# Performance work log

Measured on AMD Instinct MI355X. Metric: run time of the kernel, lower is better.

Reference implementation:

```python
import jax, jax.numpy as jnp
import numpy as np

N_ARY = 4
H_SIZE = 512
X_SIZE = 512
DEPTH = 9
N_NODES = (N_ARY ** DEPTH - 1) // (N_ARY - 1)  # 87381, complete 4-ary tree, BFS numbering


def setup_inputs() -> dict:
    key = jax.random.key(0)
    ks = jax.random.split(key, 7)
    x = jax.random.normal(ks[0], (N_NODES, X_SIZE), jnp.float32)
    # torch nn.Linear convention: y = x @ W.T + b, W:[out, in]
    Ww = jax.random.normal(ks[1], (H_SIZE, X_SIZE), jnp.float32) * (X_SIZE ** -0.5)
    Wb = jax.random.normal(ks[2], (H_SIZE,), jnp.float32) * 0.01
    Uzr_w = jax.random.normal(ks[3], (2 * H_SIZE, N_ARY * H_SIZE), jnp.float32) * ((N_ARY * H_SIZE) ** -0.5)
    Uzr_b = jax.random.normal(ks[4], (2 * H_SIZE,), jnp.float32) * 0.01
    Uh_w = jax.random.normal(ks[5], (H_SIZE, N_ARY * H_SIZE), jnp.float32) * ((N_ARY * H_SIZE) ** -0.5)
    Uh_b = jax.random.normal(ks[6], (H_SIZE,), jnp.float32) * 0.01
    return {"x": x, "Ww": Ww, "Wb": Wb, "Uzr_w": Uzr_w, "Uzr_b": Uzr_b,
            "Uh_w": Uh_w, "Uh_b": Uh_b, "depth": DEPTH}


def reference(x, Ww, Wb, Uzr_w, Uzr_b, Uh_w, Uh_b, depth):
    n_ary = N_ARY
    h_size = Ww.shape[0]
    # initial state for every node; leaves keep it, internal nodes get overwritten
    h = jnp.tanh(x @ Ww.T + Wb)  # [N, H]
    # level l occupies indices [starts[l], starts[l+1]); level 0 is the root
    starts = [(n_ary ** l - 1) // (n_ary - 1) for l in range(depth + 1)]
    # process internal levels leaves-first (deepest internal level -> root)
    for l in range(depth - 2, -1, -1):
        s, e = starts[l], starts[l + 1]
        ids = np.arange(s, e)
        child = ids[:, None] * n_ary + 1 + np.arange(n_ary)[None, :]  # [m, n_ary]
        hc = h[child]                                  # gather children: [m, n_ary, H]
        m = e - s
        h_cat = hc.reshape(m, n_ary * h_size)          # mailbox concat (full arity -> no pad)
        zr = h_cat @ Uzr_w.T + Uzr_b                   # [m, 2H]
        z = jax.nn.sigmoid(zr[:, :h_size])
        r = jax.nn.sigmoid(zr[:, h_size:])
        h_cand = jnp.tanh((jnp.tile(r, (1, n_ary)) * h_cat) @ Uh_w.T + Uh_b)
        h_new = hc.sum(axis=1) * z + (1.0 - z) * h_cand
        h = h.at[s:e].set(h_new)                       # scatter level update
    return h
```

## Files before the change

kernel.cpp:

```cpp
#include <hip/hip_runtime.h>
#include <math.h>

#define H 512
typedef unsigned short u16;
typedef __attribute__((ext_vector_type(8))) short bf16x8;
typedef __attribute__((ext_vector_type(4))) float f32x4;
typedef __attribute__((ext_vector_type(8))) unsigned short u16x8;

constexpr int LEAF0  = 21845;
constexpr int NLEAF  = 65536;
constexpr int NNODES = 87381;

__device__ __forceinline__ u16 f2b(float f) {
    union { float f; unsigned u; } v; v.f = f;
    unsigned r = v.u + 0x7fffu + ((v.u >> 16) & 1u);
    return (u16)(r >> 16);
}
__device__ __forceinline__ float b2f(u16 b) {
    union { unsigned u; float f; } v; v.u = ((unsigned)b) << 16; return v.f;
}
__device__ __forceinline__ float sigm(float x) {
    return __fdividef(1.f, 1.f + __expf(-x));
}
__device__ __forceinline__ float ftanh(float x) {
    float e = __expf(-2.f * fabsf(x));
    float r = __fdividef(1.f - e, 1.f + e);
    return copysignf(r, x);
}

template<int N> __device__ __forceinline__ void vmwait() {
    if constexpr (N == 0)        asm volatile("s_waitcnt vmcnt(0)" ::: "memory");
    else if constexpr (N == 2)   asm volatile("s_waitcnt vmcnt(2)" ::: "memory");
    else if constexpr (N == 3)   asm volatile("s_waitcnt vmcnt(3)" ::: "memory");
    else if constexpr (N == 4)   asm volatile("s_waitcnt vmcnt(4)" ::: "memory");
    else if constexpr (N == 6)   asm volatile("s_waitcnt vmcnt(6)" ::: "memory");
    else if constexpr (N == 8)   asm volatile("s_waitcnt vmcnt(8)" ::: "memory");
    else if constexpr (N == 16)  asm volatile("s_waitcnt vmcnt(16)" ::: "memory");
    else                         asm volatile("s_waitcnt vmcnt(0)" ::: "memory");
}

__device__ __forceinline__ void gload16(const u16* g, u16* l) {
    __builtin_amdgcn_global_load_lds(
        (const __attribute__((address_space(1))) void*)g,
        (__attribute__((address_space(3))) void*)l, 16, 0, 0);
}

template<int EPI, int NC, int WC>
__device__ __forceinline__ void epi_vec(
    const f32x4* va, int gr, int gc0,
    float* __restrict__ outf, u16* __restrict__ outb,
    u16* __restrict__ zrb, const u16* auxl, int lrow, int coffs, int outRow0)
{
    constexpr int NV = NC / 8;
    if constexpr (EPI == 1) {
        f32x4 ov[NC/4]; u16x8 hv[NV];
#pragma unroll
        for (int i = 0; i < NC; ++i) {
            float v = ftanh(va[i>>2][i&3]);
            ov[i>>2][i&3] = v; hv[i>>3][i&7] = f2b(v);
        }
        size_t o = (size_t)(outRow0 + gr) * H + gc0;
#pragma unroll
        for (int j = 0; j < NC/4; ++j) *(f32x4*)&outf[o + 4*j] = ov[j];
#pragma unroll
        for (int j = 0; j < NV; ++j) *(u16x8*)&outb[o + 8*j] = hv[j];
    } else if constexpr (EPI == 0) {
        auto aux_read = [&](int ch, int jj) -> u16x8 {
            int cr  = 4*lrow + ch;
            int key = (cr >> 2) & (WC/8 - 1);
            int j   = (coffs >> 3) + jj;
            return *(const u16x8*)&auxl[cr*WC + ((j ^ key) << 3)];
        };
        if (gc0 < H) {
            u16x8 zv[NV]; f32x4 hs[NC/4];
#pragma unroll
            for (int i = 0; i < NC; ++i) {
                zv[i>>3][i&7] = f2b(sigm(va[i>>2][i&3]));
                hs[i>>2][i&3] = 0.f;
            }
#pragma unroll
            for (int ch = 0; ch < 4; ++ch) {
#pragma unroll
                for (int j = 0; j < NV; ++j) {
                    u16x8 cv = aux_read(ch, j);
#pragma unroll
                    for (int k = 0; k < 8; ++k) {
                        int i = 8*j + k;
                        hs[i>>2][i&3] += b2f(cv[k]);
                    }
                }
            }
            u16x8 sv[NV];
#pragma unroll
            for (int i = 0; i < NC; ++i) sv[i>>3][i&7] = f2b(hs[i>>2][i&3]);
            size_t zo = (size_t)gr * 1024 + gc0;
#pragma unroll
            for (int j = 0; j < NV; ++j) *(u16x8*)&zrb[zo + 8*j] = zv[j];
#pragma unroll
            for (int j = 0; j < NV; ++j) *(u16x8*)&zrb[zo + H + 8*j] = sv[j];
        } else {
            f32x4 rr[NC/4];
#pragma unroll
            for (int i = 0; i < NC; ++i) rr[i>>2][i&3] = sigm(va[i>>2][i&3]);
            const int cc = gc0 - H;
#pragma unroll
            for (int ch = 0; ch < 4; ++ch) {
#pragma unroll
                for (int j = 0; j < NV; ++j) {
                    u16x8 cv = aux_read(ch, j);
                    u16x8 ov;
#pragma unroll
                    for (int k = 0; k < 8; ++k) {
                        int i = 8*j + k;
                        ov[k] = f2b(rr[i>>2][i&3] * b2f(cv[k]));
                    }
                    *(u16x8*)&outb[(size_t)gr*2048 + ch*H + cc + 8*j] = ov;
                }
            }
        }
    } else {
        size_t zo = (size_t)gr * 1024 + gc0;
        u16x8 zv[NV], sv[NV];
#pragma unroll
        for (int j = 0; j < NV; ++j) zv[j] = *(const u16x8*)&zrb[zo + 8*j];
#pragma unroll
        for (int j = 0; j < NV; ++j) sv[j] = *(const u16x8*)&zrb[zo + H + 8*j];
        f32x4 ov[NC/4]; u16x8 hv[NV];
#pragma unroll
        for (int i = 0; i < NC; ++i) {
            float hc = ftanh(va[i>>2][i&3]);
            float z  = b2f(zv[i>>3][i&7]);
            float v  = b2f(sv[i>>3][i&7]) * z + (1.f - z) * hc;
            ov[i>>2][i&3] = v; hv[i>>3][i&7] = f2b(v);
        }
        size_t o = (size_t)(outRow0 + gr) * H + gc0;
#pragma unroll
        for (int j = 0; j < NC/4; ++j) *(f32x4*)&outf[o + 4*j] = ov[j];
#pragma unroll
        for (int j = 0; j < NV; ++j) *(u16x8*)&outb[o + 8*j] = hv[j];
    }
}

template<int WC>
__device__ __forceinline__ void stage_aux(
    u16* wls, const u16* auxg, int lane)
{
    constexpr int UPW = WC / 8;
    constexpr int NIT = 64 * UPW / 64;
#pragma unroll
    for (int it = 0; it < NIT; ++it) {
        int row = (it * 64 + lane) / UPW;
        int sp  = (lane & (UPW - 1)) ^ ((row >> 2) & (UPW - 1));
        gload16(auxg + row * H + sp * 8, &wls[it * 512]);
    }
}

__global__ void cvt_all(const float* __restrict__ s0, u16* __restrict__ d0, int n0,
                        const float* __restrict__ s1, u16* __restrict__ d1, int n1,
                        const float* __restrict__ s2, u16* __restrict__ d2, int n2,
                        const float* __restrict__ s3, u16* __restrict__ d3, int n3)
{
    int i = blockIdx.x * blockDim.x + threadIdx.x;
    int st = gridDim.x * blockDim.x;
    int tot = n0 + n1 + n2 + n3;
    for (; i < tot; i += st) {
        const float* s; u16* d; int k = i;
        if (k < n0)      { s = s0; d = d0; }
        else { k -= n0;
        if (k < n1)      { s = s1; d = d1; }
        else { k -= n1;
        if (k < n2)      { s = s2; d = d2; }
        else { k -= n2;    s = s3; d = d3; } } }
        float4 v = ((const float4*)s)[k];
        ushort4 o;
        o.x = f2b(v.x); o.y = f2b(v.y); o.z = f2b(v.z); o.w = f2b(v.w);
        ((ushort4*)d)[k] = o;
    }
}

template<int EPI>
__global__ __launch_bounds__(512, 2) void gemm2c(
    const u16* __restrict__ A, int lda, int M, int K,
    const u16* __restrict__ Bm,
    const float* __restrict__ bias,
    float* __restrict__ outf,
    u16*  __restrict__ outb,
    u16*  __restrict__ zrb,
    const u16* __restrict__ auxb,
    int outRow0)
{
    constexpr int MI = 8, NI = 4;
    constexpr int AH = 256 * 32;
    constexpr int BH = 256 * 32;
    constexpr int L  = 4;

    __shared__ __align__(16) char smem[4 * (AH + BH) * 2];
    u16* Asm = reinterpret_cast<u16*>(smem);
    u16* Bsm = reinterpret_cast<u16*>(smem) + 4 * AH;

    const int tid  = threadIdx.x;
    const int lane = tid & 63;
    const int wave = tid >> 6;
    const int wm = wave >> 2;
    const int wn = wave & 3;

    int bx, by;
    {
        const int gx = gridDim.x, gy = gridDim.y;
        int p = blockIdx.y * gx + blockIdx.x;
        if ((gy & 7) == 0) {
            int xcd = p & 7, slot = p >> 3;
            bx = slot % gx;
            by = (slot / gx) * 8 + xcd;
        } else { bx = blockIdx.x; by = blockIdx.y; }
    }
    const int row0 = by * 256;
    const int col0 = bx * 256;

    const u16 *gA0, *gA1, *gB0, *gB1;
    int lA0, lA1, lB0, lB1;
    {
        int e8 = tid, row = e8 >> 2, jc = e8 & 3, js = jc ^ ((row >> 1) & 3);
        gA0 = A  + (size_t)(row0 + row) * lda + js * 8;  lA0 = e8 * 8;
        gB0 = Bm + (size_t)(col0 + row) * K   + js * 8;  lB0 = e8 * 8;
        int e9 = 512 + tid, row2 = e9 >> 2, jc2 = e9 & 3,
            js2 = jc2 ^ ((row2 >> 1) & 3);
        gA1 = A  + (size_t)(row0 + row2) * lda + js2 * 8; lA1 = e9 * 8;
        gB1 = Bm + (size_t)(col0 + row2) * K   + js2 * 8; lB1 = e9 * 8;
    }
    auto stage = [&](int slot) {
        gload16(gA0, &Asm[slot * AH + lA0]); gA0 += 32;
        gload16(gA1, &Asm[slot * AH + lA1]); gA1 += 32;
        gload16(gB0, &Bsm[slot * BH + lB0]); gB0 += 32;
        gload16(gB1, &Bsm[slot * BH + lB1]); gB1 += 32;
    };

    const int rl = lane & 15;
    const int qq = lane >> 4;
    const int ua   = qq ^ ((rl >> 1) & 3);
    const int aoff = (wm * 128 + rl) * 32 + ua * 8;
    const int boff = (wn * 64  + rl) * 32 + ua * 8;

    f32x4 acc[MI][NI] = {};
    const int nh = K / 32;

    stage(0); stage(1); stage(2);

    for (int h = 0; h < nh; ++h) {
        const int rem = nh - h;
        if (rem >= 3)      vmwait<2 * L>();
        else if (rem == 2) vmwait<L>();
        else               vmwait<0>();
        __builtin_amdgcn_s_barrier();
        asm volatile("" ::: "memory");
        if (h + 3 < nh) stage((h + 3) & 3);

        const u16* aB = Asm + (h & 3) * AH + aoff;
        const u16* bB = Bsm + (h & 3) * BH + boff;
        bf16x8 fa[MI], fb[NI];
#pragma unroll
        for (int mi = 0; mi < MI; ++mi)
            fa[mi] = *(const bf16x8*)(aB + mi * 512);
#pragma unroll
        for (int ni = 0; ni < NI; ++ni)
            fb[ni] = *(const bf16x8*)(bB + ni * 512);
        __builtin_amdgcn_s_setprio(1);
#pragma unroll
        for (int mi = 0; mi < MI; ++mi)
#pragma unroll
            for (int ni = 0; ni < NI; ++ni)
                acc[mi][ni] = __builtin_amdgcn_mfma_f32_16x16x32_bf16(
                    fa[mi], fb[ni], acc[mi][ni], 0, 0, 0);
        __builtin_amdgcn_s_setprio(0);
    }

    float bcol[NI];
#pragma unroll
    for (int ni = 0; ni < NI; ++ni)
        bcol[ni] = bias[col0 + wn * 64 + ni * 16 + rl];

    __syncthreads();
    char* wreg = smem + wave * 8192;
    float* Csw = reinterpret_cast<float*>(wreg);
    u16*   wls = reinterpret_cast<u16*>(wreg);
    const int rq  = lane >> 4;
    const int rl2 = lane & 15;
#pragma unroll
    for (int mi = 0; mi < MI; ++mi) {
#pragma unroll
        for (int ni = 0; ni < NI; ++ni)
#pragma unroll
            for (int q = 0; q < 4; ++q)
                Csw[(rq*4 + q)*68 + ni*16 + rl2] = acc[mi][ni][q] + bcol[ni];
        asm volatile("s_waitcnt lgkmcnt(0)" ::: "memory");
        f32x4 va[4];
#pragma unroll
        for (int j = 0; j < 4; ++j)
            va[j] = *(const f32x4*)&Csw[rl2*68 + rq*16 + 4*j];
        if constexpr (EPI == 0) {
            asm volatile("s_waitcnt lgkmcnt(0)" ::: "memory");
            int c0 = ((col0 < H) ? col0 : col0 - H) + wn * 64;
            const u16* auxg = auxb + (size_t)(4*(row0 + wm*128 + mi*16)) * H + c0;
            stage_aux<64>(wls, auxg, lane);
            vmwait<0>();
        }
        int gr  = row0 + wm*128 + mi*16 + rl2;
        int gc0 = col0 + wn*64 + rq*16;
        if (gr < M)
            epi_vec<EPI, 16, 64>(va, gr, gc0, outf, outb, zrb, wls, rl2, rq*16, outRow0);
    }
}

template<int EPI>
__global__ __launch_bounds__(512, 2) void gemm8p(
    const u16* __restrict__ A, int lda, int M, int K,
    const u16* __restrict__ Bm,
    const float* __restrict__ bias,
    float* __restrict__ outf,
    u16*  __restrict__ outb,
    u16*  __restrict__ zrb,
    const u16* __restrict__ auxb,
    int outRow0)
{
    constexpr int MI = 4, NI = 4;
    constexpr int AH = 256 * 32;
    constexpr int BH = 128 * 32;
    constexpr int L  = 3;

    __shared__ __align__(16) char smem[(4 * AH + 4 * BH) * 2];
    u16* Asm = reinterpret_cast<u16*>(smem);
    u16* Bsm = reinterpret_cast<u16*>(smem) + 4 * AH;

    const int tid  = threadIdx.x;
    const int lane = tid & 63;
    const int wave = tid >> 6;
    const int wm = wave >> 1;
    const int wn = wave & 1;

    int bx, by;
    {
        const int gx = gridDim.x, gy = gridDim.y;
        int p = blockIdx.y * gx + blockIdx.x;
        if ((gy & 7) == 0) {
            int xcd = p & 7, slot = p >> 3;
            bx = slot % gx;
            by = (slot / gx) * 8 + xcd;
        } else { bx = blockIdx.x; by = blockIdx.y; }
    }
    const int row0 = by * 256;
    const int col0 = bx * 128;

    const u16 *gA0, *gA1, *gB;
    int ldsA0, ldsA1, ldsB;
    {
        int e8 = tid, row = e8 >> 2, jc = e8 & 3, js = jc ^ ((row >> 1) & 3);
        gA0 = A + (size_t)(row0 + row) * lda + js * 8;  ldsA0 = e8 * 8;
        int e9 = 512 + tid, row2 = e9 >> 2, jc2 = e9 & 3,
            js2 = jc2 ^ ((row2 >> 1) & 3);
        gA1 = A + (size_t)(row0 + row2) * lda + js2 * 8; ldsA1 = e9 * 8;
        int br = tid >> 2, bjc = tid & 3, bjs = bjc ^ ((br >> 1) & 3);
        gB = Bm + (size_t)(col0 + br) * K + bjs * 8;     ldsB = tid * 8;
    }
    auto stage = [&](int slot) {
        gload16(gA0, &Asm[slot * AH + ldsA0]); gA0 += 32;
        gload16(gA1, &Asm[slot * AH + ldsA1]); gA1 += 32;
        gload16(gB,  &Bsm[slot * BH + ldsB]);  gB  += 32;
    };

    const int rl = lane & 15;
    const int qq = lane >> 4;
    const int ua   = qq ^ ((rl >> 1) & 3);
    const int aoff = (wm * 64 + rl) * 32 + ua * 8;
    const int boff = (wn * 64 + rl) * 32 + ua * 8;

    auto ld_frags = [&](int h, bf16x8 (&fa)[MI], bf16x8 (&fb)[NI]) {
        const u16* aB = Asm + (h & 3) * AH + aoff;
        const u16* bB = Bsm + (h & 3) * BH + boff;
#pragma unroll
        for (int mi = 0; mi < MI; ++mi)
            fa[mi] = *(const bf16x8*)(aB + mi * 512);
#pragma unroll
        for (int ni = 0; ni < NI; ++ni)
            fb[ni] = *(const bf16x8*)(bB + ni * 512);
    };

    f32x4 acc[MI][NI] = {};
    const int nh = K / 32;
    bf16x8 fa0[MI], fb0[NI], fa1[MI], fb1[NI];

    stage(0); stage(1); stage(2);
    vmwait<2 * L>();
    __builtin_amdgcn_s_barrier();
    asm volatile("" ::: "memory");
    ld_frags(0, fa0, fb0);

    auto iter = [&](int h, bf16x8 (&cfa)[MI], bf16x8 (&cfb)[NI],
                           bf16x8 (&nfa)[MI], bf16x8 (&nfb)[NI]) {
        if (h + 2 < nh) vmwait<L>();
        else            vmwait<0>();
        __builtin_amdgcn_s_barrier();
        asm volatile("" ::: "memory");
        if (h + 3 < nh) stage((h + 3) & 3);
        if (h + 1 < nh) ld_frags(h + 1, nfa, nfb);
        __builtin_amdgcn_s_setprio(1);
#pragma unroll
        for (int mi = 0; mi < MI; ++mi)
#pragma unroll
            for (int ni = 0; ni < NI; ++ni)
                acc[mi][ni] = __builtin_amdgcn_mfma_f32_16x16x32_bf16(
                    cfa[mi], cfb[ni], acc[mi][ni], 0, 0, 0);
        __builtin_amdgcn_s_setprio(0);
    };

    for (int h = 0; h < nh; h += 2) {
        iter(h,     fa0, fb0, fa1, fb1);
        iter(h + 1, fa1, fb1, fa0, fb0);
    }

    float bcol[NI];
#pragma unroll
    for (int ni = 0; ni < NI; ++ni)
        bcol[ni] = bias[col0 + wn * 64 + ni * 16 + rl];

    __syncthreads();
    char* wreg = smem + wave * 8192;
    float* Csw = reinterpret_cast<float*>(wreg);
    u16*   wls = reinterpret_cast<u16*>(wreg);
    const int rq  = lane >> 4;
    const int rl2 = lane & 15;
#pragma unroll
    for (int mi = 0; mi < MI; ++mi) {
#pragma unroll
        for (int ni = 0; ni < NI; ++ni)
#pragma unroll
            for (int q = 0; q < 4; ++q)
                Csw[(rq*4 + q)*68 + ni*16 + rl2] = acc[mi][ni][q] + bcol[ni];
        asm volatile("s_waitcnt lgkmcnt(0)" ::: "memory");
        f32x4 va[4];
#pragma unroll
        for (int j = 0; j < 4; ++j)
            va[j] = *(const f32x4*)&Csw[rl2*68 + rq*16 + 4*j];
        if constexpr (EPI == 0) {
            asm volatile("s_waitcnt lgkmcnt(0)" ::: "memory");
            int c0 = ((col0 < H) ? col0 : col0 - H) + wn * 64;
            const u16* auxg = auxb + (size_t)(4*(row0 + wm*64 + mi*16)) * H + c0;
            stage_aux<64>(wls, auxg, lane);
            vmwait<0>();
        }
        int gr  = row0 + wm*64 + mi*16 + rl2;
        int gc0 = col0 + wn*64 + rq*16;
        if (gr < M)
            epi_vec<EPI, 16, 64>(va, gr, gc0, outf, outb, zrb, wls, rl2, rq*16, outRow0);
    }
}

template<int EPI>
__global__ __launch_bounds__(512) void gemm512(
    const u16* __restrict__ A, int lda, int M, int K,
    const u16* __restrict__ Bm,
    const float* __restrict__ bias,
    float* __restrict__ outf,
    u16*  __restrict__ outb,
    u16*  __restrict__ zrb,
    const u16* __restrict__ auxb,
    int outRow0)
{
    __shared__ __align__(16) char smem[4*128*32*2 * 2];
    u16* Asm = reinterpret_cast<u16*>(smem);
    u16* Bsm = reinterpret_cast<u16*>(smem) + 4 * 128 * 32;

    const int tid  = threadIdx.x;
    const int lane = tid & 63;
    const int wave = tid >> 6;
    const int wm = wave >> 2;
    const int wn = wave & 3;

    int bx, by;
    {
        const int gx = gridDim.x, gy = gridDim.y;
        int p = blockIdx.y * gx + blockIdx.x;
        if ((gy & 7) == 0) {
            int xcd = p & 7, slot = p >> 3;
            bx = slot % gx;
            by = (slot / gx) * 8 + xcd;
        } else { bx = blockIdx.x; by = blockIdx.y; }
    }
    const int row0 = by * 128;
    const int col0 = bx * 128;

    const u16 *gA, *gB;
    int ldsE;
    {
        int row = tid >> 2, jc = tid & 3, js = jc ^ ((row >> 1) & 3);
        gA = A  + (size_t)(row0 + row) * lda + js * 8;
        gB = Bm + (size_t)(col0 + row) * K   + js * 8;
        ldsE = tid * 8;
    }
    auto stage = [&](int b) {
        gload16(gA, &Asm[b * (128*32) + ldsE]); gA += 32;
        gload16(gB, &Bsm[b * (128*32) + ldsE]); gB += 32;
    };

    const int rl = lane & 15;
    const int qq = lane >> 4;
    const int ua   = qq ^ ((rl >> 1) & 3);
    const int aoff = (wm * 64 + rl) * 32 + ua * 8;
    const int boff = (wn * 32 + rl) * 32 + ua * 8;

    f32x4 acc[4][2] = {};
    const int nt = K / 32;
    stage(0);
    stage(1);

    for (int t = 0; t < nt; ++t) {
        if (t + 2 < nt) {
            stage((t + 2) & 3);
            vmwait<4>();
        } else if (t + 2 == nt) {
            vmwait<2>();
        } else {
            vmwait<0>();
        }
        __builtin_amdgcn_s_barrier();
        asm volatile("" ::: "memory");

        const u16* aB = Asm + (t & 3) * (128*32) + aoff;
        const u16* bB = Bsm + (t & 3) * (128*32) + boff;
        bf16x8 af[4], bfr[2];
#pragma unroll
        for (int mi = 0; mi < 4; ++mi)
            af[mi] = *(const bf16x8*)(aB + mi * 512);
#pragma unroll
        for (int ni = 0; ni < 2; ++ni)
            bfr[ni] = *(const bf16x8*)(bB + ni * 512);
#pragma unroll
        for (int mi = 0; mi < 4; ++mi)
#pragma unroll
            for (int ni = 0; ni < 2; ++ni)
                acc[mi][ni] = __builtin_amdgcn_mfma_f32_16x16x32_bf16(
                    af[mi], bfr[ni], acc[mi][ni], 0, 0, 0);
    }

    float bcol[2];
#pragma unroll
    for (int ni = 0; ni < 2; ++ni)
        bcol[ni] = bias[col0 + wn * 32 + ni * 16 + rl];

    __syncthreads();
    char* wreg = smem + wave * 8192;
    float* Csw = reinterpret_cast<float*>(wreg);
    u16*   wls = reinterpret_cast<u16*>(wreg);
    const int rq  = lane >> 4;
    const int rl2 = lane & 15;
#pragma unroll
    for (int mi = 0; mi < 4; ++mi) {
#pragma unroll
        for (int ni = 0; ni < 2; ++ni)
#pragma unroll
            for (int q = 0; q < 4; ++q)
                Csw[(rq*4 + q)*36 + ni*16 + rl2] = acc[mi][ni][q] + bcol[ni];
        asm volatile("s_waitcnt lgkmcnt(0)" ::: "memory");
        f32x4 va[2];
#pragma unroll
        for (int j = 0; j < 2; ++j)
            va[j] = *(const f32x4*)&Csw[rl2*36 + rq*8 + 4*j];
        if constexpr (EPI == 0) {
            asm volatile("s_waitcnt lgkmcnt(0)" ::: "memory");
            int c0 = ((col0 < H) ? col0 : col0 - H) + wn * 32;
            const u16* auxg = auxb + (size_t)(4*(row0 + wm*64 + mi*16)) * H + c0;
            stage_aux<32>(wls, auxg, lane);
            vmwait<0>();
        }
        int gr  = row0 + wm*64 + mi*16 + rl2;
        int gc0 = col0 + wn*32 + rq*8;
        if (gr < M)
            epi_vec<EPI, 8, 32>(va, gr, gc0, outf, outb, zrb, wls, rl2, rq*8, outRow0);
    }
}

template<int EPI>
__global__ __launch_bounds__(256, 1) void gemm_sk(
    const u16* __restrict__ A, int lda, int M, int K,
    const u16* __restrict__ Bm,
    const float* __restrict__ bias,
    float* __restrict__ outf,
    u16*  __restrict__ outb,
    u16*  __restrict__ zrb,
    const u16* __restrict__ auxb,
    int outRow0)
{
    __shared__ __align__(16) char smem[98304];
    u16* ring = reinterpret_cast<u16*>(smem);

    const int tid  = threadIdx.x;
    const int lane = tid & 63;
    const int wave = tid >> 6;
    const int row0 = blockIdx.y * 64;
    const int col0 = blockIdx.x * 64;
    const int KC   = K >> 2;
    const int kb0  = wave * KC;
    const int NS   = KC / 32;

    u16* wring = ring + wave * 12288;

    auto stage = [&](int sl, int kt) {
        u16* As = wring + sl * 4096;
        u16* Bs = As + 2048;
#pragma unroll
        for (int it = 0; it < 4; ++it) {
            int e8  = it * 64 + lane;
            int row = e8 >> 2;
            int jc  = e8 & 3;
            int js  = jc ^ ((row >> 1) & 3);
            int ar = row0 + row; if (ar >= M) ar = M - 1;
            gload16(A + (size_t)ar * lda + kt + js * 8, &As[e8 * 8]);
            gload16(Bm + (size_t)(col0 + row) * K + kt + js * 8, &Bs[e8 * 8]);
        }
    };

    const int rl = lane & 15;
    const int qq = lane >> 4;
    const int ua   = qq ^ ((rl >> 1) & 3);
    const int aoff = rl * 32 + ua * 8;

    f32x4 acc[4][4] = {};
    stage(0, kb0);
    stage(1, kb0 + 32);

    for (int s = 0; s < NS; ++s) {
        if (s + 2 < NS) { stage((s + 2) % 3, kb0 + (s + 2) * 32); vmwait<16>(); }
        else if (s + 1 < NS) vmwait<8>();
        else                 vmwait<0>();
        asm volatile("" ::: "memory");
        const u16* As = wring + (s % 3) * 4096;
        const u16* Bs = As + 2048;
        bf16x8 af[4], bfr[4];
#pragma unroll
        for (int mi = 0; mi < 4; ++mi)
            af[mi] = *(const bf16x8*)&As[aoff + mi * 512];
#pragma unroll
        for (int ni = 0; ni < 4; ++ni)
            bfr[ni] = *(const bf16x8*)&Bs[aoff + ni * 512];
#pragma unroll
        for (int mi = 0; mi < 4; ++mi)
#pragma unroll
            for (int ni = 0; ni < 4; ++ni)
                acc[mi][ni] = __builtin_amdgcn_mfma_f32_16x16x32_bf16(
                    af[mi], bfr[ni], acc[mi][ni], 0, 0, 0);
    }

    __syncthreads();
    float* P  = reinterpret_cast<float*>(smem);
    float* Pw = P + wave * 4096;
    const int rq = lane >> 4;
#pragma unroll
    for (int mi = 0; mi < 4; ++mi)
#pragma unroll
        for (int ni = 0; ni < 4; ++ni)
#pragma unroll
            for (int q = 0; q < 4; ++q)
                Pw[(mi*16 + rq*4 + q) * 64 + ni*16 + rl] = acc[mi][ni][q];
    asm volatile("s_waitcnt lgkmcnt(0)" ::: "memory");
    __syncthreads();

    u16* auxl = reinterpret_cast<u16*>(smem + 65536);
    if constexpr (EPI == 0) {
        int c0 = (col0 < H) ? col0 : col0 - H;
        const u16* auxg = auxb + (size_t)(4 * row0) * H + c0;
        const int maxr = 4 * (M - row0);
#pragma unroll
        for (int it = 0; it < 8; ++it) {
            int e   = it * 256 + tid;
            int row = e >> 3;
            int crow = row; if (crow >= maxr) crow = maxr - 1;
            int sp  = (e & 7) ^ ((row >> 2) & 7);
            gload16(auxg + (size_t)crow * H + sp * 8, &auxl[e * 8]);
        }
    }

    const int orow = tid >> 2;
    const int cq   = tid & 3;
    f32x4 va[4];
#pragma unroll
    for (int j = 0; j < 4; ++j) {
        f32x4 v = *(const f32x4*)&P[orow*64 + cq*16 + 4*j];
#pragma unroll
        for (int w = 1; w < 4; ++w)
            v += *(const f32x4*)&P[w*4096 + orow*64 + cq*16 + 4*j];
        v += *(const f32x4*)&bias[col0 + cq*16 + 4*j];
        va[j] = v;
    }
    if constexpr (EPI == 0) vmwait<0>();
    asm volatile("s_waitcnt lgkmcnt(0)" ::: "memory");
    int gr = row0 + orow;
    if (gr < M)
        epi_vec<EPI, 16, 64>(va, gr, col0 + cq*16, outf, outb, zrb,
                             auxl, orow, cq*16, outRow0);
}

extern "C" void kernel_launch(void* const* d_in, const int* in_sizes, int n_in,
                              void* d_out, int out_size, void* d_ws, size_t ws_size,
                              hipStream_t stream) {
    const float* x     = (const float*)d_in[0];
    const float* Ww    = (const float*)d_in[1];
    const float* Wb    = (const float*)d_in[2];
    const float* Uzr_w = (const float*)d_in[3];
    const float* Uzr_b = (const float*)d_in[4];
    const float* Uh_w  = (const float*)d_in[5];
    const float* Uh_b  = (const float*)d_in[6];
    float* out = (float*)d_out;

    char* ws = (char*)d_ws;
    size_t off = 0;
    u16* hb   = (u16*)(ws + off); off += (size_t)NNODES * H * 2;
    u16* zr   = (u16*)(ws + off); off += (size_t)16384 * 1024 * 2;
    u16* rhxb = (u16*)(ws + off); off += (size_t)16384 * 2048 * 2;
    u16* Wwb  = (u16*)(ws + off); off += (size_t)512 * 512 * 2;
    u16* Uzrb = (u16*)(ws + off); off += (size_t)1024 * 2048 * 2;
    u16* Uhb  = (u16*)(ws + off); off += (size_t)512 * 2048 * 2;

    cvt_all<<<dim3(8192), 256, 0, stream>>>(
        Ww, Wwb, 512 * 512 / 4,
        Uzr_w, Uzrb, 1024 * 2048 / 4,
        Uh_w, Uhb, 512 * 2048 / 4,
        x + (size_t)LEAF0 * H, rhxb, NLEAF * H / 4);

    gemm2c<1><<<dim3(H / 256, NLEAF / 256), 512, 0, stream>>>(
        rhxb, H, NLEAF, H, Wwb, Wb, out, hb, nullptr, nullptr, LEAF0);

    static const int pow4[9] = {1, 4, 16, 64, 256, 1024, 4096, 16384, 65536};
    int starts[10]; starts[0] = 0;
    for (int l = 0; l < 9; ++l) starts[l + 1] = starts[l] + pow4[l];

    for (int l = 7; l >= 0; --l) {
        int s = starts[l], m = pow4[l];
        int cs = 4 * s + 1;
        if (m >= 16384) {
            gemm2c<0><<<dim3(1024 / 256, m / 256), 512, 0, stream>>>(
                hb + (size_t)cs * H, 2048, m, 2048, Uzrb, Uzr_b,
                nullptr, rhxb, zr, hb + (size_t)cs * H, 0);
            gemm8p<2><<<dim3(H / 128, m / 256), 512, 0, stream>>>(
                rhxb, 2048, m, 2048, Uhb, Uh_b,
                out, hb, zr, nullptr, s);
        } else if (m >= 4096) {
            int gm = (m + 127) / 128;
            gemm512<0><<<dim3(1024 / 128, gm), 512, 0, stream>>>(
                hb + (size_t)cs * H, 2048, m, 2048, Uzrb, Uzr_b,
                nullptr, rhxb, zr, hb + (size_t)cs * H, 0);
            gemm512<2><<<dim3(H / 128, gm), 512, 0, stream>>>(
                rhxb, 2048, m, 2048, Uhb, Uh_b,
                out, hb, zr, nullptr, s);
        } else {
            int gm = (m + 63) / 64;
            gemm_sk<0><<<dim3(1024 / 64, gm), 256, 0, stream>>>(
                hb + (size_t)cs * H, 2048, m, 2048, Uzrb, Uzr_b,
                nullptr, rhxb, zr, hb + (size_t)cs * H, 0);
            gemm_sk<2><<<dim3(512 / 64, gm), 256, 0, stream>>>(
                rhxb, 2048, m, 2048, Uhb, Uh_b,
                out, hb, zr, nullptr, s);
        }
    }
}
```

Baseline: 475.9 us.

## Replace large-level GEMMs with 128x128 double-buffered 256-thread kernel

Adds a new GEMM kernel with 128x128 tiles, 4 waves, a two-stage LDS double buffer and up to three blocks per CU, and uses it for both the zr and candidate GEMMs on the 16384-node level. It replaces the 256x256 and 256x128 tile kernels that used 4-slot deep pipelines and held fragments for the next step in registers. Smaller tiles give more blocks and better occupancy for an M of 16384, but lower data reuse per tile and a shallower prefetch that waits on all loads every iteration.

```diff
diff --git a/kernel.cpp b/kernel.cpp
--- a/kernel.cpp
+++ b/kernel.cpp
@@ -179,6 +179,133 @@
 }
 
 template<int EPI>
+__global__ __launch_bounds__(256, 3) void gemm97(
+    const u16* __restrict__ A, int lda, int M, int K,
+    const u16* __restrict__ Bm,
+    const float* __restrict__ bias,
+    float* __restrict__ outf,
+    u16*  __restrict__ outb,
+    u16*  __restrict__ zrb,
+    const u16* __restrict__ auxb,
+    int outRow0)
+{
+    constexpr int TS = 128 * 32;
+
+    __shared__ __align__(16) char smem[2 * 2 * TS * 2];
+    u16* Asm = reinterpret_cast<u16*>(smem);
+    u16* Bsm = reinterpret_cast<u16*>(smem) + 2 * TS;
+
+    const int tid  = threadIdx.x;
+    const int lane = tid & 63;
+    const int wave = tid >> 6;
+    const int wm = wave >> 1;
+    const int wn = wave & 1;
+
+    int bx, by;
+    {
+        const int gx = gridDim.x, gy = gridDim.y;
+        int p = blockIdx.y * gx + blockIdx.x;
+        if ((gy & 7) == 0) {
+            int xcd = p & 7, slot = p >> 3;
+            bx = slot % gx;
+            by = (slot / gx) * 8 + xcd;
+        } else { bx = blockIdx.x; by = blockIdx.y; }
+    }
+    const int row0 = by * 128;
+    const int col0 = bx * 128;
+
+    const u16 *gA[2], *gB[2];
+    int lA[2], lB[2];
+#pragma unroll
+    for (int j = 0; j < 2; ++j) {
+        int e8 = j * 256 + tid;
+        int row = e8 >> 2, jc = e8 & 3, js = jc ^ ((row >> 1) & 3);
+        int ar = row0 + row; if (ar >= M) ar = M - 1;
+        gA[j] = A  + (size_t)ar * lda + js * 8;          lA[j] = e8 * 8;
+        gB[j] = Bm + (size_t)(col0 + row) * K + js * 8;  lB[j] = e8 * 8;
+    }
+    auto stage = [&](int b) {
+#pragma unroll
+        for (int j = 0; j < 2; ++j) {
+            gload16(gA[j], &Asm[b * TS + lA[j]]); gA[j] += 32;
+            gload16(gB[j], &Bsm[b * TS + lB[j]]); gB[j] += 32;
+        }
+    };
+
+    const int rl = lane & 15;
+    const int qq = lane >> 4;
+    const int ua   = qq ^ ((rl >> 1) & 3);
+    const int aoff = (wm * 64 + rl) * 32 + ua * 8;
+    const int boff = (wn * 64 + rl) * 32 + ua * 8;
+
+    f32x4 acc[4][4] = {};
+    const int nt = K / 32;
+
+    stage(0);
+
+    for (int t = 0; t < nt; ++t) {
+        vmwait<0>();
+        __builtin_amdgcn_s_barrier();
+        asm volatile("" ::: "memory");
+        if (t + 1 < nt) stage((t + 1) & 1);
+
+        const u16* aB = Asm + (t & 1) * TS + aoff;
+        const u16* bB = Bsm + (t & 1) * TS + boff;
+        bf16x8 af[4], bfr[4];
+#pragma unroll
+        for (int mi = 0; mi < 4; ++mi)
+            af[mi] = *(const bf16x8*)(aB + mi * 512);
+#pragma unroll
+        for (int ni = 0; ni < 4; ++ni)
+            bfr[ni] = *(const bf16x8*)(bB + ni * 512);
+        __builtin_amdgcn_s_setprio(1);
+#pragma unroll
+        for (int mi = 0; mi < 4; ++mi)
+#pragma unroll
+            for (int ni = 0; ni < 4; ++ni)
+                acc[mi][ni] = __builtin_amdgcn_mfma_f32_16x16x32_bf16(
+                    af[mi], bfr[ni], acc[mi][ni], 0, 0, 0);
+        __builtin_amdgcn_s_setprio(0);
+    }
+
+    float bcol[4];
+#pragma unroll
+    for (int ni = 0; ni < 4; ++ni)
+        bcol[ni] = bias[col0 + wn * 64 + ni * 16 + rl];
+
+    __syncthreads();
+    char* wreg = smem + wave * 8192;
+    float* Csw = reinterpret_cast<float*>(wreg);
+    u16*   wls = reinterpret_cast<u16*>(wreg);
+    const int rq  = lane >> 4;
+    const int rl2 = lane & 15;
+#pragma unroll
+    for (int mi = 0; mi < 4; ++mi) {
+#pragma unroll
+        for (int ni = 0; ni < 4; ++ni)
+#pragma unroll
+            for (int q = 0; q < 4; ++q)
+                Csw[(rq*4 + q)*68 + ni*16 + rl2] = acc[mi][ni][q] + bcol[ni];
+        asm volatile("s_waitcnt lgkmcnt(0)" ::: "memory");
+        f32x4 va[4];
+#pragma unroll
+        for (int j = 0; j < 4; ++j)
+            va[j] = *(const f32x4*)&Csw[rl2*68 + rq*16 + 4*j];
+        if constexpr (EPI == 0) {
+            asm volatile("s_waitcnt lgkmcnt(0)" ::: "memory");
+            int c0 = ((col0 < H) ? col0 : col0 - H) + wn * 64;
+            const u16* auxg = auxb + (size_t)(4*(row0 + wm*64 + mi*16)) * H + c0;
+            stage_aux<64>(wls, auxg, lane);
+            vmwait<0>();
+        }
+        int gr  = row0 + wm*64 + mi*16 + rl2;
+        int gc0 = col0 + wn*64 + rq*16;
+        if (gr < M)
+            epi_vec<EPI, 16, 64>(va, gr, gc0, outf, outb, zrb, wls, rl2, rq*16, outRow0);
+    }
+}
+
+template<int EPI>
 __global__ __launch_bounds__(512, 2) void gemm2c(
     const u16* __restrict__ A, int lda, int M, int K,
     const u16* __restrict__ Bm,
@@ -312,149 +439,6 @@
 }
 
 template<int EPI>
-__global__ __launch_bounds__(512, 2) void gemm8p(
-    const u16* __restrict__ A, int lda, int M, int K,
-    const u16* __restrict__ Bm,
-    const float* __restrict__ bias,
-    float* __restrict__ outf,
-    u16*  __restrict__ outb,
-    u16*  __restrict__ zrb,
-    const u16* __restrict__ auxb,
-    int outRow0)
-{
-    constexpr int MI = 4, NI = 4;
-    constexpr int AH = 256 * 32;
-    constexpr int BH = 128 * 32;
-    constexpr int L  = 3;
-
-    __shared__ __align__(16) char smem[(4 * AH + 4 * BH) * 2];
-    u16* Asm = reinterpret_cast<u16*>(smem);
-    u16* Bsm = reinterpret_cast<u16*>(smem) + 4 * AH;
-
-    const int tid  = threadIdx.x;
-    const int lane = tid & 63;
-    const int wave = tid >> 6;
-    const int wm = wave >> 1;
-    const int wn = wave & 1;
-
-    int bx, by;
-    {
-        const int gx = gridDim.x, gy = gridDim.y;
-        int p = blockIdx.y * gx + blockIdx.x;
-        if ((gy & 7) == 0) {
-            int xcd = p & 7, slot = p >> 3;
-            bx = slot % gx;
-            by = (slot / gx) * 8 + xcd;
-        } else { bx = blockIdx.x; by = blockIdx.y; }
-    }
-    const int row0 = by * 256;
-    const int col0 = bx * 128;
-
-    const u16 *gA0, *gA1, *gB;
-    int ldsA0, ldsA1, ldsB;
-    {
-        int e8 = tid, row = e8 >> 2, jc = e8 & 3, js = jc ^ ((row >> 1) & 3);
-        gA0 = A + (size_t)(row0 + row) * lda + js * 8;  ldsA0 = e8 * 8;
-        int e9 = 512 + tid, row2 = e9 >> 2, jc2 = e9 & 3,
-            js2 = jc2 ^ ((row2 >> 1) & 3);
-        gA1 = A + (size_t)(row0 + row2) * lda + js2 * 8; ldsA1 = e9 * 8;
-        int br = tid >> 2, bjc = tid & 3, bjs = bjc ^ ((br >> 1) & 3);
-        gB = Bm + (size_t)(col0 + br) * K + bjs * 8;     ldsB = tid * 8;
-    }
-    auto stage = [&](int slot) {
-        gload16(gA0, &Asm[slot * AH + ldsA0]); gA0 += 32;
-        gload16(gA1, &Asm[slot * AH + ldsA1]); gA1 += 32;
-        gload16(gB,  &Bsm[slot * BH + ldsB]);  gB  += 32;
-    };
-
-    const int rl = lane & 15;
-    const int qq = lane >> 4;
-    const int ua   = qq ^ ((rl >> 1) & 3);
-    const int aoff = (wm * 64 + rl) * 32 + ua * 8;
-    const int boff = (wn * 64 + rl) * 32 + ua * 8;
-
-    auto ld_frags = [&](int h, bf16x8 (&fa)[MI], bf16x8 (&fb)[NI]) {
-        const u16* aB = Asm + (h & 3) * AH + aoff;
-        const u16* bB = Bsm + (h & 3) * BH + boff;
-#pragma unroll
-        for (int mi = 0; mi < MI; ++mi)
-            fa[mi] = *(const bf16x8*)(aB + mi * 512);
-#pragma unroll
-        for (int ni = 0; ni < NI; ++ni)
-            fb[ni] = *(const bf16x8*)(bB + ni * 512);
-    };
-
-    f32x4 acc[MI][NI] = {};
-    const int nh = K / 32;
-    bf16x8 fa0[MI], fb0[NI], fa1[MI], fb1[NI];
-
-    stage(0); stage(1); stage(2);
-    vmwait<2 * L>();
-    __builtin_amdgcn_s_barrier();
-    asm volatile("" ::: "memory");
-    ld_frags(0, fa0, fb0);
-
-    auto iter = [&](int h, bf16x8 (&cfa)[MI], bf16x8 (&cfb)[NI],
-                           bf16x8 (&nfa)[MI], bf16x8 (&nfb)[NI]) {
-        if (h + 2 < nh) vmwait<L>();
-        else            vmwait<0>();
-        __builtin_amdgcn_s_barrier();
-        asm volatile("" ::: "memory");
-        if (h + 3 < nh) stage((h + 3) & 3);
-        if (h + 1 < nh) ld_frags(h + 1, nfa, nfb);
-        __builtin_amdgcn_s_setprio(1);
-#pragma unroll
-        for (int mi = 0; mi < MI; ++mi)
-#pragma unroll
-            for (int ni = 0; ni < NI; ++ni)
-                acc[mi][ni] = __builtin_amdgcn_mfma_f32_16x16x32_bf16(
-                    cfa[mi], cfb[ni], acc[mi][ni], 0, 0, 0);
-        __builtin_amdgcn_s_setprio(0);
-    };
-
-    for (int h = 0; h < nh; h += 2) {
-        iter(h,     fa0, fb0, fa1, fb1);
-        iter(h + 1, fa1, fb1, fa0, fb0);
-    }
-
-    float bcol[NI];
-#pragma unroll
-    for (int ni = 0; ni < NI; ++ni)
-        bcol[ni] = bias[col0 + wn * 64 + ni * 16 + rl];
-
-    __syncthreads();
-    char* wreg = smem + wave * 8192;
-    float* Csw = reinterpret_cast<float*>(wreg);
-    u16*   wls = reinterpret_cast<u16*>(wreg);
-    const int rq  = lane >> 4;
-    const int rl2 = lane & 15;
-#pragma unroll
-    for (int mi = 0; mi < MI; ++mi) {
-#pragma unroll
-        for (int ni = 0; ni < NI; ++ni)
-#pragma unroll
-            for (int q = 0; q < 4; ++q)
-                Csw[(rq*4 + q)*68 + ni*16 + rl2] = acc[mi][ni][q] + bcol[ni];
-        asm volatile("s_waitcnt lgkmcnt(0)" ::: "memory");
-        f32x4 va[4];
-#pragma unroll
-        for (int j = 0; j < 4; ++j)
-            va[j] = *(const f32x4*)&Csw[rl2*68 + rq*16 + 4*j];
-        if constexpr (EPI == 0) {
-            asm volatile("s_waitcnt lgkmcnt(0)" ::: "memory");
-            int c0 = ((col0 < H) ? col0 : col0 - H) + wn * 64;
-            const u16* auxg = auxb + (size_t)(4*(row0 + wm*64 + mi*16)) * H + c0;
-            stage_aux<64>(wls, auxg, lane);
-            vmwait<0>();
-        }
-        int gr  = row0 + wm*64 + mi*16 + rl2;
-        int gc0 = col0 + wn*64 + rq*16;
-        if (gr < M)
-            epi_vec<EPI, 16, 64>(va, gr, gc0, outf, outb, zrb, wls, rl2, rq*16, outRow0);
-    }
-}
-
-template<int EPI>
 __global__ __launch_bounds__(512) void gemm512(
     const u16* __restrict__ A, int lda, int M, int K,
     const u16* __restrict__ Bm,
@@ -736,10 +720,10 @@
         int s = starts[l], m = pow4[l];
         int cs = 4 * s + 1;
         if (m >= 16384) {
-            gemm2c<0><<<dim3(1024 / 256, m / 256), 512, 0, stream>>>(
+            gemm97<0><<<dim3(1024 / 128, m / 128), 256, 0, stream>>>(
                 hb + (size_t)cs * H, 2048, m, 2048, Uzrb, Uzr_b,
                 nullptr, rhxb, zr, hb + (size_t)cs * H, 0);
-            gemm8p<2><<<dim3(H / 128, m / 256), 512, 0, stream>>>(
+            gemm97<2><<<dim3(H / 128, m / 128), 256, 0, stream>>>(
                 rhxb, 2048, m, 2048, Uhb, Uh_b,
                 out, hb, zr, nullptr, s);
         } else if (m >= 4096) {
```

Measured after the change: 494.1 us. 3.8% more time.
